# Optimization experiments

Hardware: AMD Instinct MI355X
Metric: run time of the kernel (lower is better)

## Reference

```python
import jax, jax.numpy as jnp
import numpy as np

WS = 8
NH = 16
EPS = 1e-5

# relative position index (static, same as the torch buffer)
def _rel_index(ws):
    coords = np.stack(np.meshgrid(np.arange(ws), np.arange(ws), indexing='ij'))  # 2,ws,ws
    flat = coords.reshape(2, -1)
    rel = flat[:, :, None] - flat[:, None, :]
    rel = rel.transpose(1, 2, 0).copy()
    rel[..., 0] += ws - 1
    rel[..., 1] += ws - 1
    rel[..., 0] *= 2 * ws - 1
    return rel.sum(-1)  # (ws*ws, ws*ws)

REL_IDX = jnp.asarray(_rel_index(WS))

def conv2d(x, w, dilation=1, pad=None, groups=1):
    k = w.shape[-1]
    if pad is None:
        pad = (dilation * (k - 1)) // 2
    return jax.lax.conv_general_dilated(
        x, w, (1, 1), ((pad, pad), (pad, pad)), rhs_dilation=(dilation, dilation),
        dimension_numbers=('NCHW', 'OIHW', 'NCHW'), feature_group_count=groups)

def bn(x, p):
    g, b, m, v = p[0], p[1], p[2], p[3]
    inv = g / jnp.sqrt(v + EPS)
    return x * inv[:, None, None] + (b - m * inv)[:, None, None]

def avgpool(x, kh, kw, ph, pw):
    # torch AvgPool2d with count_include_pad=True: zero-pad then divide by kernel size
    s = jax.lax.reduce_window(x, 0.0, jax.lax.add, (1, 1, kh, kw), (1, 1, 1, 1),
                              ((0, 0), (0, 0), (ph, ph), (pw, pw)))
    return s / (kh * kw)

def _fwd(x, w_pre, bn_pre, w_l1, bn_l1, w_l2, bn_l2, w_l3, bn_l3, w_qkv, rpb, w_dw, w_pw, bn_proj):
    B, C, H, W = x.shape
    # local conv branch (chunk 256 -> 86,86,84 with dilations 1,2,3)
    local = bn(conv2d(x, w_pre), bn_pre)
    l1 = bn(conv2d(local[:, :86], w_l1, dilation=1), bn_l1)
    l2 = bn(conv2d(local[:, 86:172], w_l2, dilation=2), bn_l2)
    l3 = bn(conv2d(local[:, 172:], w_l3, dilation=3), bn_l3)
    local = jnp.concatenate([l1, l2, l3], axis=1)
    # pad to window multiple (reflect); static shapes so Python branch is fine
    ph, pw = (-H) % WS, (-W) % WS
    if ph or pw:
        x = jnp.pad(x, ((0, 0), (0, 0), (0, ph), (0, pw)), mode='reflect')
    Hp, Wp = H + ph, W + pw
    hh, ww = Hp // WS, Wp // WS
    d = C // NH
    qkv = conv2d(x, w_qkv)  # (B, 3C, Hp, Wp)
    qkv = qkv.reshape(B, 3, NH, d, hh, WS, ww, WS)
    qkv = qkv.transpose(1, 0, 4, 6, 2, 5, 7, 3).reshape(3, B * hh * ww, NH, WS * WS, d)
    q, k, v = qkv[0], qkv[1], qkv[2]
    dots = jnp.einsum('whid,whjd->whij', q, k) * (d ** -0.5)
    bias = rpb[REL_IDX.reshape(-1)].reshape(WS * WS, WS * WS, NH).transpose(2, 0, 1)
    attn = jax.nn.softmax(dots + bias[None], axis=-1)
    out = jnp.einsum('whij,whjd->whid', attn, v)
    out = out.reshape(B, hh, ww, NH, WS, WS, d).transpose(0, 3, 6, 1, 4, 2, 5).reshape(B, C, Hp, Wp)
    out = out[:, :, :H, :W]
    ax = avgpool(jnp.pad(out, ((0, 0), (0, 0), (0, 1), (0, 0)), mode='reflect'), WS, 1, WS // 2 - 1, 0)
    ay = avgpool(jnp.pad(out, ((0, 0), (0, 0), (0, 0), (0, 1)), mode='reflect'), 1, WS, 0, WS // 2 - 1)
    out = ax + ay + local
    out = jnp.pad(out, ((0, 0), (0, 0), (0, 1), (0, 1)), mode='reflect')
    out = conv2d(out, w_dw, pad=3, groups=C)       # depthwise 8x8
    out = bn(conv2d(out, w_pw), bn_proj)           # pointwise + BN
    return out[:, :, :H, :W]

def setup_inputs() -> dict:
    key = jax.random.key(0)
    ks = jax.random.split(key, 16)
    def w(k, shape, s=0.05):
        return jax.random.normal(k, shape, dtype=jnp.float32) * s
    def bnp(k, c):
        p = jax.random.uniform(k, (4, c), dtype=jnp.float32)
        return p.at[3].add(0.5)  # keep var positive and away from 0
    return {
        'x': jax.random.normal(ks[0], (8, 256, 128, 128), dtype=jnp.float32),
        'w_pre': w(ks[1], (256, 256, 1, 1)), 'bn_pre': bnp(ks[2], 256),
        'w_l1': w(ks[3], (86, 86, 3, 3)), 'bn_l1': bnp(ks[4], 86),
        'w_l2': w(ks[5], (86, 86, 3, 3)), 'bn_l2': bnp(ks[6], 86),
        'w_l3': w(ks[7], (84, 84, 3, 3)), 'bn_l3': bnp(ks[8], 84),
        'w_qkv': w(ks[9], (768, 256, 1, 1)),
        'rpb': w(ks[10], (225, 16), 0.02),
        'w_dw': w(ks[11], (256, 1, 8, 8)),
        'w_pw': w(ks[12], (256, 256, 1, 1)),
        'bn_proj': bnp(ks[13], 256),
    }

def reference(x, w_pre, bn_pre, w_l1, bn_l1, w_l2, bn_l2, w_l3, bn_l3, w_qkv, rpb, w_dw, w_pw, bn_proj):
    return _fwd(x, w_pre, bn_pre, w_l1, bn_l1, w_l2, bn_l2, w_l3, bn_l3, w_qkv, rpb, w_dw, w_pw, bn_proj)
```

## Files before the change

### kernel.cpp

```cpp
#include <hip/hip_runtime.h>
#include <hip/hip_bf16.h>
#include <cstdint>
#include <cstddef>

namespace {

constexpr int HW = 16384;

typedef short vec8s __attribute__((ext_vector_type(8)));
typedef float f32x4 __attribute__((ext_vector_type(4)));

__device__ __forceinline__ float u2f(uint32_t u){ union { uint32_t u; float f; } v; v.u = u; return v.f; }
__device__ __forceinline__ uint32_t f2u(float f){ union { float f; uint32_t u; } v; v.f = f; return v.u; }
__device__ __forceinline__ uint16_t f2bf(float f){
  uint32_t u = f2u(f);
  u += 0x7fffu + ((u >> 16) & 1u);
  return (uint16_t)(u >> 16);
}
__device__ __forceinline__ void unpack2(uint32_t w, float& lo, float& hi){
  lo = u2f(w << 16);
  hi = u2f(w & 0xffff0000u);
}

__global__ __launch_bounds__(256) void k_cast(
    const float* __restrict__ x, uint16_t* __restrict__ xT)
{
  __shared__ float sF[64][129];
  const int t = threadIdx.x;
  const int b = blockIdx.x >> 7;
  const int y = blockIdx.x & 127;
  const size_t rowoff = (size_t)y * 128;
  for (int cc = 0; cc < 4; ++cc) {
    const int cic0 = cc * 64;
    #pragma unroll
    for (int k = 0; k < 8; ++k) {
      int e = t + k * 256;
      int ci = e >> 5;
      int pxq = (e & 31) * 4;
      float4 v = *(const float4*)(x + (size_t)(b * 256 + cic0 + ci) * HW + rowoff + pxq);
      sF[ci][pxq] = v.x; sF[ci][pxq+1] = v.y; sF[ci][pxq+2] = v.z; sF[ci][pxq+3] = v.w;
    }
    __syncthreads();
    {
      int px = t >> 1, h = t & 1;
      __align__(16) uint16_t tmp[32];
      #pragma unroll
      for (int j = 0; j < 32; ++j) tmp[j] = f2bf(sF[h * 32 + j][px]);
      uint16_t* dst = xT + ((size_t)b * HW + rowoff + px) * 256 + cic0 + h * 32;
      *(uint4*)(dst)      = *(uint4*)&tmp[0];
      *(uint4*)(dst + 8)  = *(uint4*)&tmp[8];
      *(uint4*)(dst + 16) = *(uint4*)&tmp[16];
      *(uint4*)(dst + 24) = *(uint4*)&tmp[24];
    }
    __syncthreads();
  }
}

template<int OUT_MODE, int NCO>
__global__ __launch_bounds__(256) void k_gemm_v2(
    const uint16_t* __restrict__ xT, const float* __restrict__ wmat,
    const float* __restrict__ bnp, int M,
    uint16_t* __restrict__ outb, float* __restrict__ outf)
{
  __shared__ __align__(16) uint16_t sX[128][260];
  __shared__ __align__(16) uint16_t sW[128][36];
  const int t = threadIdx.x;
  const int b    = blockIdx.x >> 7;
  const int tile = blockIdx.x & 127;
  const int l = t & 63, w = t >> 6;
  const int l15 = l & 15, koct = l >> 4;
  const int wc = w >> 1, wp = w & 1;

  {
    const int spx = t >> 1, sh = t & 1;
    int gpx;
    if constexpr (OUT_MODE == 3) {
      int win = tile * 2 + (spx >> 6);
      int p = spx & 63;
      gpx = ((win >> 4) * 8 + (p >> 3)) * 128 + (win & 15) * 8 + (p & 7);
    } else {
      gpx = tile * 128 + spx;
    }
    const uint16_t* src = xT + ((size_t)b * HW + gpx) * 256 + sh * 128;
    uint16_t* dst = &sX[spx][sh * 128];
    #pragma unroll
    for (int i = 0; i < 16; ++i)
      *(uint4*)(dst + i * 8) = *(const uint4*)(src + i * 8);
  }

  const int swc = t >> 1, swh = t & 1;
  float4 wr0, wr1, wr2, wr3;
  {
    const float* p = wmat + (size_t)swc * 256 + swh * 16;
    wr0 = *(const float4*)(p);     wr1 = *(const float4*)(p + 4);
    wr2 = *(const float4*)(p + 8); wr3 = *(const float4*)(p + 12);
  }
  __syncthreads();

  for (int cc = 0; cc < NCO; ++cc) {
    f32x4 acc[4][4];
    #pragma unroll
    for (int cf = 0; cf < 4; ++cf)
      #pragma unroll
      for (int pf = 0; pf < 4; ++pf) acc[cf][pf] = (f32x4){0.f,0.f,0.f,0.f};

    for (int kc = 0; kc < 8; ++kc) {
      if (cc | kc) __syncthreads();
      {
        __align__(16) uint16_t tmp[16];
        tmp[0]=f2bf(wr0.x); tmp[1]=f2bf(wr0.y); tmp[2]=f2bf(wr0.z); tmp[3]=f2bf(wr0.w);
        tmp[4]=f2bf(wr1.x); tmp[5]=f2bf(wr1.y); tmp[6]=f2bf(wr1.z); tmp[7]=f2bf(wr1.w);
        tmp[8]=f2bf(wr2.x); tmp[9]=f2bf(wr2.y); tmp[10]=f2bf(wr2.z); tmp[11]=f2bf(wr2.w);
        tmp[12]=f2bf(wr3.x); tmp[13]=f2bf(wr3.y); tmp[14]=f2bf(wr3.z); tmp[15]=f2bf(wr3.w);
        uint16_t* dst = &sW[swc][swh * 16];
        *(uint4*)(dst)     = *(uint4*)&tmp[0];
        *(uint4*)(dst + 8) = *(uint4*)&tmp[8];
      }
      {
        int nkc = kc + 1, ncc = cc;
        if (nkc == 8) { nkc = 0; ncc = cc + 1; }
        if (ncc < NCO) {
          const float* p = wmat + (size_t)(ncc * 128 + swc) * 256 + nkc * 32 + swh * 16;
          wr0 = *(const float4*)(p);     wr1 = *(const float4*)(p + 4);
          wr2 = *(const float4*)(p + 8); wr3 = *(const float4*)(p + 12);
        }
      }
      __syncthreads();
      vec8s bf[4];
      #pragma unroll
      for (int pf = 0; pf < 4; ++pf)
        bf[pf] = *(const vec8s*)&sX[wp * 64 + pf * 16 + l15][kc * 32 + koct * 8];
      #pragma unroll
      for (int cf = 0; cf < 4; ++cf) {
        vec8s af = *(const vec8s*)&sW[wc * 64 + cf * 16 + l15][koct * 8];
        #pragma unroll
        for (int pf = 0; pf < 4; ++pf)
          acc[cf][pf] = __builtin_amdgcn_mfma_f32_16x16x32_bf16(af, bf[pf], acc[cf][pf], 0, 0, 0);
      }
    }

    #pragma unroll
    for (int cf = 0; cf < 4; ++cf) {
      const int cbase = cc * 128 + wc * 64 + cf * 16 + koct * 4;
      float scv[4], shv[4];
      #pragma unroll
      for (int r = 0; r < 4; ++r) {
        scv[r] = 1.f; shv[r] = 0.f;
        if constexpr (OUT_MODE == 0 || OUT_MODE == 2) {
          int c = cbase + r;
          float g = bnp[c], be = bnp[M + c], mu = bnp[2 * M + c], va = bnp[3 * M + c];
          scv[r] = g * rsqrtf(va + 1e-5f);
          shv[r] = be - mu * scv[r];
        }
      }
      #pragma unroll
      for (int pf = 0; pf < 4; ++pf) {
        if constexpr (OUT_MODE == 0) {
          int px = tile * 128 + wp * 64 + pf * 16 + l15;
          __align__(8) uint16_t pk[4];
          #pragma unroll
          for (int r = 0; r < 4; ++r)
            pk[r] = f2bf(fmaf(acc[cf][pf][r], scv[r], shv[r]));
          *(uint2*)(outb + ((size_t)b * HW + px) * 256 + cbase) = *(uint2*)pk;
        } else if constexpr (OUT_MODE == 2) {
          int px = tile * 128 + wp * 64 + pf * 16 + l15;
          #pragma unroll
          for (int r = 0; r < 4; ++r)
            outf[(size_t)(b * M + cbase + r) * HW + px] =
                fmaf(acc[cf][pf][r], scv[r], shv[r]);
        } else {
          int win = tile * 2 + wp;
          int p = pf * 16 + l15;
          uint16_t* dstp = outb + ((size_t)(b * 256 + win) * 768 + cbase) * 64 + p;
          #pragma unroll
          for (int r = 0; r < 4; ++r)
            dstp[(size_t)r * 64] = f2bf(acc[cf][pf][r]);
        }
      }
    }
  }
}

template<int DIL, int CG>
__global__ __launch_bounds__(256) void k_dilconv_mfma(
    const uint16_t* __restrict__ preT, const float* __restrict__ wt,
    const float* __restrict__ bnp, float* __restrict__ out,
    int cb, int cb_al)
{
  constexpr int R = 8 + 2 * DIL;
  constexpr int C = 64 + 2 * DIL;
  constexpr int NPOS = R * C;
  constexpr int NIT = (NPOS + 255) / 256;
  __shared__ __align__(16) uint16_t sX[NPOS * 16];
  __shared__ __align__(16) uint16_t sW[10 * 50 * 16];

  const int t = threadIdx.x;
  const int rt    = blockIdx.x >> 1;
  const int ctile = blockIdx.x & 1;
  const int ct2   = blockIdx.y;
  const int b     = blockIdx.z;
  const int y0 = rt * 8, x0 = ctile * 64;
  const int l = t & 63, w = t >> 6;
  const int l15 = l & 15, oct = (l >> 4) & 1, half = l >> 5;
  const int rbase = w * 2;

  f32x4 acc[3][8];
  #pragma unroll
  for (int cf = 0; cf < 3; ++cf)
    #pragma unroll
    for (int q = 0; q < 8; ++q) acc[cf][q] = (f32x4){0.f,0.f,0.f,0.f};

  for (int kc = 0; kc < 6; ++kc) {
    #pragma unroll
    for (int i = 0; i < 3; ++i) {
      int pair = t + i * 256;
      int co = pair >> 4, ci = pair & 15;
      int cog = ct2 * 48 + co;
      int c = cb_al + kc * 16 + ci;
      bool ok = (cog < CG) && (c >= cb) && (c < cb + CG);
      size_t widx = ok ? ((size_t)cog * (size_t)CG + (size_t)(c - cb)) * 9u
                       : (size_t)0;
      const float* wp = wt + widx;
      uint16_t* dst = &sW[co * 16 + ci];
      #pragma unroll
      for (int tap = 0; tap < 9; ++tap)
        dst[tap * 800] = ok ? f2bf(wp[tap]) : (uint16_t)0;
      dst[9 * 800] = 0;
    }
    #pragma unroll
    for (int i = 0; i < NIT; ++i) {
      int p = t + i * 256;
      if (p < NPOS) {
        int row = p / C, col = p % C;
        int gy = y0 + row - DIL, gx = x0 + col - DIL;
        uint4 va = {0,0,0,0}, vb = {0,0,0,0};
        if ((unsigned)gy < 128u && (unsigned)gx < 128u) {
          const uint4* src = (const uint4*)(preT +
              (((size_t)b * HW + gy * 128 + gx) * 256 + cb_al + kc * 16));
          va = src[0]; vb = src[1];
        }
        uint4* dst = (uint4*)&sX[p * 16];
        dst[0] = va; dst[1] = vb;
      }
    }
    __syncthreads();

    #pragma unroll
    for (int s = 0; s < 5; ++s) {
      const int tap0 = 2 * s, tap1 = 2 * s + 1;
      const int dy0 = tap0 / 3, dx0 = tap0 % 3;
      const int dy1 = (tap1 <= 8) ? tap1 / 3 : 2;
      const int dx1 = (tap1 <= 8) ? tap1 % 3 : 2;
      const int dy = half ? dy1 : dy0;
      const int dx = half ? dx1 : dx0;
      const int atap = tap0 + half;
      vec8s a0 = *(const vec8s*)&sW[(atap * 50 + 0  + l15) * 16 + oct * 8];
      vec8s a1 = *(const vec8s*)&sW[(atap * 50 + 16 + l15) * 16 + oct * 8];
      vec8s a2 = *(const vec8s*)&sW[(atap * 50 + 32 + l15) * 16 + oct * 8];
      #pragma unroll
      for (int rs = 0; rs < 2; ++rs) {
        const int rowin = rbase + rs + dy * DIL;
        #pragma unroll
        for (int c4 = 0; c4 < 4; ++c4) {
          const int colin = c4 * 16 + l15 + dx * DIL;
          vec8s bf = *(const vec8s*)&sX[(rowin * C + colin) * 16 + oct * 8];
          acc[0][rs*4+c4] = __builtin_amdgcn_mfma_f32_16x16x32_bf16(a0, bf, acc[0][rs*4+c4], 0, 0, 0);
          acc[1][rs*4+c4] = __builtin_amdgcn_mfma_f32_16x16x32_bf16(a1, bf, acc[1][rs*4+c4], 0, 0, 0);
          acc[2][rs*4+c4] = __builtin_amdgcn_mfma_f32_16x16x32_bf16(a2, bf, acc[2][rs*4+c4], 0, 0, 0);
        }
      }
    }
    __syncthreads();
  }

  const int row4 = (l >> 4);
  #pragma unroll
  for (int cf = 0; cf < 3; ++cf) {
    #pragma unroll
    for (int r = 0; r < 4; ++r) {
      int c_loc = ct2 * 48 + cf * 16 + row4 * 4 + r;
      if (c_loc < CG) {
        int cg = cb + c_loc;
        float g = bnp[c_loc], be = bnp[CG + c_loc];
        float mu = bnp[2 * CG + c_loc], va = bnp[3 * CG + c_loc];
        float scv = g * rsqrtf(va + 1e-5f);
        float shv = be - mu * scv;
        #pragma unroll
        for (int rs = 0; rs < 2; ++rs) {
          int y = y0 + rbase + rs;
          #pragma unroll
          for (int c4 = 0; c4 < 4; ++c4) {
            int x = x0 + c4 * 16 + l15;
            out[(size_t)(b * 256 + cg) * HW + y * 128 + x] =
                fmaf(acc[cf][rs*4+c4][r], scv, shv);
          }
        }
      }
    }
  }
}

__global__ __launch_bounds__(256) void k_attn(
    const uint16_t* __restrict__ qkvW, const float* __restrict__ rpb,
    uint16_t* __restrict__ outp)
{
  __shared__ __align__(16) uint16_t sAll[4][9928];
  const int t = threadIdx.x;
  const int l = t & 63, w = t >> 6;
  const int l15 = l & 15, koct = l >> 4;
  const int b = blockIdx.y;
  const int win = blockIdx.x;
  const int wy = win >> 4, wx = win & 15;
  const int wbase = (wy * 8) * 128 + wx * 8;
  const uint16_t* base = qkvW + (size_t)(b * 256 + win) * 49152;
  uint16_t* swKT = &sAll[w][0];
  uint16_t* swQT = &sAll[w][2560];
  uint16_t* swPT = &sAll[w][5120];
  float*    swB  = (float*)&sAll[w][9472];
  float*    swO  = (float*)swPT;

  {
    uint4 z = {0,0,0,0};
    *(uint4*)(swKT + l * 40 + 16) = z;
    *(uint4*)(swKT + l * 40 + 24) = z;
    *(uint4*)(swQT + l * 40 + 16) = z;
    *(uint4*)(swQT + l * 40 + 24) = z;
  }

  for (int it = 0; it < 4; ++it) {
    const int n = w + it * 4;
    #pragma unroll
    for (int m = 0; m < 4; ++m) {
      int e = l + m * 64;
      if (e < 225) swB[e] = rpb[e * 16 + n];
    }
    const uint16_t* qg = base + (size_t)(n * 16) * 64;
    const uint16_t* kg = base + (size_t)(256 + n * 16) * 64;
    const uint16_t* vg = base + (size_t)(512 + n * 16) * 64;
    {
      uint32_t kp[8], qp[8];
      #pragma unroll
      for (int m = 0; m < 8; ++m) {
        uint32_t k0 = kg[(2 * m) * 64 + l], k1 = kg[(2 * m + 1) * 64 + l];
        uint32_t q0 = qg[(2 * m) * 64 + l], q1 = qg[(2 * m + 1) * 64 + l];
        kp[m] = k0 | (k1 << 16);
        qp[m] = q0 | (q1 << 16);
      }
      *(uint4*)(swKT + l * 40)     = *(uint4*)&kp[0];
      *(uint4*)(swKT + l * 40 + 8) = *(uint4*)&kp[4];
      *(uint4*)(swQT + l * 40)     = *(uint4*)&qp[0];
      *(uint4*)(swQT + l * 40 + 8) = *(uint4*)&qp[4];
    }
    asm volatile("s_waitcnt lgkmcnt(0)" ::: "memory");
    __builtin_amdgcn_sched_barrier(0);

    vec8s aK[4], bQ[4];
    #pragma unroll
    for (int tt = 0; tt < 4; ++tt) {
      aK[tt] = *(const vec8s*)(swKT + (tt * 16 + l15) * 40 + koct * 8);
      bQ[tt] = *(const vec8s*)(swQT + (tt * 16 + l15) * 40 + koct * 8);
    }
    f32x4 accS[4][4];
    #pragma unroll
    for (int ti = 0; ti < 4; ++ti)
      #pragma unroll
      for (int tj = 0; tj < 4; ++tj)
        accS[ti][tj] = __builtin_amdgcn_mfma_f32_16x16x32_bf16(
            aK[tj], bQ[ti], (f32x4){0.f, 0.f, 0.f, 0.f}, 0, 0, 0);

    float p[4][16], sinv[4];
    #pragma unroll
    for (int ti = 0; ti < 4; ++ti) {
      const int i = ti * 16 + l15;
      const int irow = i >> 3, icol = i & 7;
      #pragma unroll
      for (int tj = 0; tj < 4; ++tj) {
        #pragma unroll
        for (int r = 0; r < 4; ++r) {
          int j = tj * 16 + koct * 4 + r;
          int rel = (irow - (j >> 3) + 7) * 15 + (icol - (j & 7) + 7);
          p[ti][tj * 4 + r] = fmaf(accS[ti][tj][r], 0.25f, swB[rel]);
        }
      }
      float mx = p[ti][0];
      #pragma unroll
      for (int u = 1; u < 16; ++u) mx = fmaxf(mx, p[ti][u]);
      mx = fmaxf(mx, __shfl_xor(mx, 16));
      mx = fmaxf(mx, __shfl_xor(mx, 32));
      float s = 0.f;
      #pragma unroll
      for (int u = 0; u < 16; ++u) { p[ti][u] = __expf(p[ti][u] - mx); s += p[ti][u]; }
      s += __shfl_xor(s, 16);
      s += __shfl_xor(s, 32);
      sinv[ti] = 1.f / s;
    }

    #pragma unroll
    for (int ti = 0; ti < 4; ++ti) {
      uint16_t* rowp = swPT + (ti * 16 + l15) * 68 + koct * 4;
      #pragma unroll
      for (int tj = 0; tj < 4; ++tj) {
        uint32_t u0 = (uint32_t)f2bf(p[ti][tj * 4 + 0]) | ((uint32_t)f2bf(p[ti][tj * 4 + 1]) << 16);
        uint32_t u1 = (uint32_t)f2bf(p[ti][tj * 4 + 2]) | ((uint32_t)f2bf(p[ti][tj * 4 + 3]) << 16);
        *(uint32_t*)(rowp + tj * 16)     = u0;
        *(uint32_t*)(rowp + tj * 16 + 2) = u1;
      }
    }
    asm volatile("s_waitcnt lgkmcnt(0)" ::: "memory");
    __builtin_amdgcn_sched_barrier(0);

    f32x4 accO[4];
    #pragma unroll
    for (int ii = 0; ii < 4; ++ii) accO[ii] = (f32x4){0.f, 0.f, 0.f, 0.f};
    #pragma unroll
    for (int ks = 0; ks < 2; ++ks) {
      vec8s aV = *(const vec8s*)(vg + l15 * 64 + ks * 32 + koct * 8);
      #pragma unroll
      for (int ii = 0; ii < 4; ++ii) {
        vec8s bP;
        const uint16_t* src = swPT + (ii * 16 + l15) * 68 + ks * 32 + koct * 8;
        *(uint2*)&bP         = *(const uint2*)(src);
        *((uint2*)&bP + 1)   = *(const uint2*)(src + 4);
        accO[ii] = __builtin_amdgcn_mfma_f32_16x16x32_bf16(aV, bP, accO[ii], 0, 0, 0);
      }
    }
    asm volatile("s_waitcnt lgkmcnt(0)" ::: "memory");
    __builtin_amdgcn_sched_barrier(0);

    #pragma unroll
    for (int ii = 0; ii < 4; ++ii) {
      #pragma unroll
      for (int r = 0; r < 4; ++r) {
        int dd = koct * 4 + r;
        swO[dd * 76 + ii * 16 + l15] = accO[ii][r] * sinv[ii];
      }
    }
    asm volatile("s_waitcnt lgkmcnt(0)" ::: "memory");
    __builtin_amdgcn_sched_barrier(0);
    #pragma unroll
    for (int e2 = 0; e2 < 2; ++e2) {
      int e = l + e2 * 64;
      int dd = e >> 3, row = e & 7;
      const float* orow = swO + dd * 76 + row * 8;
      float4 a = *(const float4*)(orow);
      float4 c = *(const float4*)(orow + 4);
      uint4 pk;
      pk.x = (uint32_t)f2bf(a.x) | ((uint32_t)f2bf(a.y) << 16);
      pk.y = (uint32_t)f2bf(a.z) | ((uint32_t)f2bf(a.w) << 16);
      pk.z = (uint32_t)f2bf(c.x) | ((uint32_t)f2bf(c.y) << 16);
      pk.w = (uint32_t)f2bf(c.z) | ((uint32_t)f2bf(c.w) << 16);
      *(uint4*)(outp + (size_t)(b * 256 + n * 16 + dd) * HW + wbase + row * 128) = pk;
    }
    asm volatile("s_waitcnt lgkmcnt(0)" ::: "memory");
    __builtin_amdgcn_sched_barrier(0);
  }
}

__global__ __launch_bounds__(256) void k_pool(
    const uint16_t* __restrict__ attnb, float* __restrict__ loc)
{
  __shared__ __align__(16) float sP[71][136];
  const int t = threadIdx.x;
  const int plane = blockIdx.x >> 1;
  const int h0 = (blockIdx.x & 1) * 64;
  const size_t pbase = (size_t)plane * HW;
  #pragma unroll
  for (int k = 0; k < 5; ++k) {
    int idx = t + k * 256;
    if (idx < 71 * 16) {
      int lr = idx >> 4, m = idx & 15;
      int g = h0 - 3 + lr;
      float f[8] = {0.f,0.f,0.f,0.f,0.f,0.f,0.f,0.f};
      if (g >= 0 && g <= 127) {
        uint4 v4 = *(const uint4*)(attnb + pbase + (size_t)g * 128 + m * 8);
        unpack2(v4.x, f[0], f[1]); unpack2(v4.y, f[2], f[3]);
        unpack2(v4.z, f[4], f[5]); unpack2(v4.w, f[6], f[7]);
      }
      float* dst = &sP[lr][4 + m * 8];
      *(float4*)dst       = (float4){f[0], f[1], f[2], f[3]};
      *(float4*)(dst + 4) = (float4){f[4], f[5], f[6], f[7]};
    }
  }
  #pragma unroll
  for (int k = 0; k < 3; ++k) {
    int idx = t + k * 256;
    if (idx < 71 * 8) {
      int lr = idx >> 3, e = idx & 7;
      int c = (e < 4) ? e : (128 + e);
      sP[lr][c] = 0.f;
    }
  }
  __syncthreads();

  const int q  = t & 31;
  const int r0 = (t >> 5) * 8;
  const int w0 = q * 4;
  float4 av = {0.f, 0.f, 0.f, 0.f};
  #pragma unroll
  for (int o = 0; o < 8; ++o) {
    float4 v = *(const float4*)&sP[r0 + o][4 + w0];
    av.x += v.x; av.y += v.y; av.z += v.z; av.w += v.w;
  }
  #pragma unroll
  for (int rr = 0; rr < 8; ++rr) {
    const int lh = r0 + rr;
    const int h = h0 + lh;
    float4 a = av;
    if (h >= 124) {
      float4 cfix = *(const float4*)&sP[126 - 64 + 3][4 + w0];
      a.x += cfix.x; a.y += cfix.y; a.z += cfix.z; a.w += cfix.w;
    }
    float4 hv0 = *(const float4*)&sP[lh + 3][w0];
    float4 hv1 = *(const float4*)&sP[lh + 3][w0 + 4];
    float4 hv2 = *(const float4*)&sP[lh + 3][w0 + 8];
    float s0 = hv0.y + hv0.z + hv0.w + hv1.x + hv1.y + hv1.z + hv1.w + hv2.x;
    float s1 = s0 - hv0.y + hv2.y;
    float s2 = s1 - hv0.z + hv2.z;
    float s3 = s2 - hv0.w + hv2.w;
    if (q == 31) {
      float cfix = sP[lh + 3][130];
      s0 += cfix; s1 += cfix; s2 += cfix; s3 += cfix;
    }
    const size_t gi = pbase + (size_t)h * 128 + w0;
    float4 lv = *(const float4*)(loc + gi);
    float4 o4;
    o4.x = fmaf(a.x + s0, 0.125f, lv.x);
    o4.y = fmaf(a.y + s1, 0.125f, lv.y);
    o4.z = fmaf(a.z + s2, 0.125f, lv.z);
    o4.w = fmaf(a.w + s3, 0.125f, lv.w);
    *(float4*)(loc + gi) = o4;
    if (rr < 7) {
      float4 vm = *(const float4*)&sP[lh][4 + w0];
      float4 vp = *(const float4*)&sP[lh + 8][4 + w0];
      av.x += vp.x - vm.x; av.y += vp.y - vm.y;
      av.z += vp.z - vm.z; av.w += vp.w - vm.w;
    }
  }
}

__global__ __launch_bounds__(256) void k_dw(
    const float* __restrict__ comb, const float* __restrict__ wdw,
    float* __restrict__ out)
{
  __shared__ __align__(16) float sZ[71][136];
  __shared__ float sWd[64];
  const int t = threadIdx.x;
  const int plane = blockIdx.x >> 1;
  const int cch = plane & 255;
  const int h0 = (blockIdx.x & 1) * 64;
  const size_t pbase = (size_t)plane * HW;
  if (t < 64) sWd[t] = wdw[cch * 64 + t];
  #pragma unroll
  for (int k = 0; k < 5; ++k) {
    int idx = t + k * 256;
    if (idx < 71 * 16) {
      int lr = idx >> 4, m = idx & 15;
      int g = h0 - 3 + lr;
      float4 a = {0.f,0.f,0.f,0.f}, c = {0.f,0.f,0.f,0.f};
      if (g >= 0 && g <= 128) {
        int gr = (g == 128) ? 126 : g;
        const float* src = comb + pbase + (size_t)gr * 128 + m * 8;
        a = *(const float4*)(src);
        c = *(const float4*)(src + 4);
      }
      float* dst = &sZ[lr][4 + m * 8];
      *(float4*)dst       = a;
      *(float4*)(dst + 4) = c;
    }
  }
  if (t < 71) {
    int lr = t;
    int g = h0 - 3 + lr;
    float rv = 0.f;
    if (g >= 0 && g <= 128) {
      int gr = (g == 128) ? 126 : g;
      rv = comb[pbase + (size_t)gr * 128 + 126];
    }
    *(float4*)&sZ[lr][0] = (float4){0.f, 0.f, 0.f, 0.f};
    sZ[lr][132] = rv;
    sZ[lr][133] = 0.f; sZ[lr][134] = 0.f; sZ[lr][135] = 0.f;
  }
  __syncthreads();

  float wt[8][8];
  #pragma unroll
  for (int i = 0; i < 8; ++i) {
    *(float4*)&wt[i][0] = *(const float4*)&sWd[i * 8];
    *(float4*)&wt[i][4] = *(const float4*)&sWd[i * 8 + 4];
  }

  const int q  = t & 31;
  const int rg = t >> 5;
  const int w0 = q * 4;
  f32x4 acc[8];
  #pragma unroll
  for (int rr = 0; rr < 8; ++rr) acc[rr] = (f32x4){0.f,0.f,0.f,0.f};

  #pragma unroll
  for (int v = 0; v < 15; ++v) {
    const int lr = rg * 8 + v;
    float win[12];
    *(float4*)&win[0] = *(const float4*)&sZ[lr][w0];
    *(float4*)&win[4] = *(const float4*)&sZ[lr][w0 + 4];
    *(float4*)&win[8] = *(const float4*)&sZ[lr][w0 + 8];
    #pragma unroll
    for (int rr = 0; rr < 8; ++rr) {
      const int i = v - rr;
      if (i >= 0 && i < 8) {
        #pragma unroll
        for (int c = 0; c < 4; ++c) {
          float s = acc[rr][c];
          #pragma unroll
          for (int j = 0; j < 8; ++j)
            s = fmaf(wt[i][j], win[c + j + 1], s);
          acc[rr][c] = s;
        }
      }
    }
  }
  #pragma unroll
  for (int rr = 0; rr < 8; ++rr) {
    int h = h0 + rg * 8 + rr;
    float* dst = out + pbase + (size_t)h * 128 + w0;
    *(float4*)dst = (float4){acc[rr][0], acc[rr][1], acc[rr][2], acc[rr][3]};
  }
}

}

extern "C" void kernel_launch(void* const* d_in, const int* in_sizes, int n_in,
                              void* d_out, int out_size, void* d_ws, size_t ws_size,
                              hipStream_t stream)
{
  const float* x      = (const float*)d_in[0];
  const float* w_pre  = (const float*)d_in[1];
  const float* bn_pre = (const float*)d_in[2];
  const float* w_l1   = (const float*)d_in[3];
  const float* bn_l1  = (const float*)d_in[4];
  const float* w_l2   = (const float*)d_in[5];
  const float* bn_l2  = (const float*)d_in[6];
  const float* w_l3   = (const float*)d_in[7];
  const float* bn_l3  = (const float*)d_in[8];
  const float* w_qkv  = (const float*)d_in[9];
  const float* rpb    = (const float*)d_in[10];
  const float* w_dw   = (const float*)d_in[11];
  const float* w_pw   = (const float*)d_in[12];
  const float* bn_pj  = (const float*)d_in[13];
  float* out = (float*)d_out;

  char* base = (char*)d_ws;
  uint16_t* xT    = (uint16_t*)base;
  uint16_t* preT  = (uint16_t*)(base + (size_t)67108864);
  float*    bufB  = (float*)(base + (size_t)134217728);
  uint16_t* bufQ  = (uint16_t*)(base + (size_t)268435456);
  uint16_t* attnO = preT;
  float*    bufDw = (float*)bufQ;
  uint16_t* dwT   = xT;

  dim3 blk(256);
  k_cast<<<dim3(1024), blk, 0, stream>>>(x, xT);
  k_gemm_v2<0, 2><<<dim3(1024), blk, 0, stream>>>(xT, w_pre, bn_pre, 256, preT, nullptr);
  k_dilconv_mfma<1, 86><<<dim3(32, 2, 8), blk, 0, stream>>>(preT, w_l1, bn_l1, bufB, 0, 0);
  k_dilconv_mfma<2, 86><<<dim3(32, 2, 8), blk, 0, stream>>>(preT, w_l2, bn_l2, bufB, 86, 80);
  k_dilconv_mfma<3, 84><<<dim3(32, 2, 8), blk, 0, stream>>>(preT, w_l3, bn_l3, bufB, 172, 160);
  k_gemm_v2<3, 6><<<dim3(1024), blk, 0, stream>>>(xT, w_qkv, nullptr, 768, bufQ, nullptr);
  k_attn<<<dim3(256, 8), blk, 0, stream>>>(bufQ, rpb, attnO);
  k_pool<<<dim3(4096), blk, 0, stream>>>(attnO, bufB);
  k_dw<<<dim3(4096), blk, 0, stream>>>(bufB, w_dw, bufDw);
  k_cast<<<dim3(1024), blk, 0, stream>>>(bufDw, dwT);
  k_gemm_v2<2, 2><<<dim3(1024), blk, 0, stream>>>(dwT, w_pw, bn_pj, 256, nullptr, out);

  (void)in_sizes; (void)n_in; (void)out_size; (void)ws_size;
}
```

Measured before the change: 761.2 us.

## Pre-convert 1x1 conv weights to bf16 and read MFMA operands from global

Adds a small kernel that casts the pre, qkv and projection 1x1 weights to bf16 once per call, storing them in scratch space (the output buffer and a freed workspace region). The GEMM kernel then loads its A fragments straight from global/L2 instead of staging converted weights through shared memory. This removes the per-k-step conversion, the shared-memory writes and two barriers per k-chunk, so the inner loop runs without synchronisation. In exchange, every wave issues its own redundant global loads of weights, relying on cache hits, and there are extra small launches.

```diff
diff --git a/kernel.cpp b/kernel.cpp
--- a/kernel.cpp
+++ b/kernel.cpp
@@ -20,6 +20,22 @@
 __device__ __forceinline__ void unpack2(uint32_t w, float& lo, float& hi){
   lo = u2f(w << 16);
   hi = u2f(w & 0xffff0000u);
+}
+
+__global__ __launch_bounds__(256) void k_w2bf(
+    const float* __restrict__ src, uint16_t* __restrict__ dst, int n)
+{
+  int i = (blockIdx.x * 256 + threadIdx.x) * 8;
+  if (i + 8 <= n) {
+    float4 a = *(const float4*)(src + i);
+    float4 b = *(const float4*)(src + i + 4);
+    uint4 pk;
+    pk.x = (uint32_t)f2bf(a.x) | ((uint32_t)f2bf(a.y) << 16);
+    pk.y = (uint32_t)f2bf(a.z) | ((uint32_t)f2bf(a.w) << 16);
+    pk.z = (uint32_t)f2bf(b.x) | ((uint32_t)f2bf(b.y) << 16);
+    pk.w = (uint32_t)f2bf(b.z) | ((uint32_t)f2bf(b.w) << 16);
+    *(uint4*)(dst + i) = pk;
+  }
 }
 
 __global__ __launch_bounds__(256) void k_cast(
@@ -57,13 +73,12 @@
 }
 
 template<int OUT_MODE, int NCO>
-__global__ __launch_bounds__(256) void k_gemm_v2(
-    const uint16_t* __restrict__ xT, const float* __restrict__ wmat,
+__global__ __launch_bounds__(256) void k_gemm_v3(
+    const uint16_t* __restrict__ xT, const uint16_t* __restrict__ wbf,
     const float* __restrict__ bnp, int M,
     uint16_t* __restrict__ outb, float* __restrict__ outf)
 {
   __shared__ __align__(16) uint16_t sX[128][260];
-  __shared__ __align__(16) uint16_t sW[128][36];
   const int t = threadIdx.x;
   const int b    = blockIdx.x >> 7;
   const int tile = blockIdx.x & 127;
@@ -87,14 +102,6 @@
     for (int i = 0; i < 16; ++i)
       *(uint4*)(dst + i * 8) = *(const uint4*)(src + i * 8);
   }
-
-  const int swc = t >> 1, swh = t & 1;
-  float4 wr0, wr1, wr2, wr3;
-  {
-    const float* p = wmat + (size_t)swc * 256 + swh * 16;
-    wr0 = *(const float4*)(p);     wr1 = *(const float4*)(p + 4);
-    wr2 = *(const float4*)(p + 8); wr3 = *(const float4*)(p + 12);
-  }
   __syncthreads();
 
   for (int cc = 0; cc < NCO; ++cc) {
@@ -104,35 +111,16 @@
       #pragma unroll
       for (int pf = 0; pf < 4; ++pf) acc[cf][pf] = (f32x4){0.f,0.f,0.f,0.f};
 
+    const uint16_t* wbase = wbf + (size_t)(cc * 128 + wc * 64 + l15) * 256 + koct * 8;
+    #pragma unroll
     for (int kc = 0; kc < 8; ++kc) {
-      if (cc | kc) __syncthreads();
-      {
-        __align__(16) uint16_t tmp[16];
-        tmp[0]=f2bf(wr0.x); tmp[1]=f2bf(wr0.y); tmp[2]=f2bf(wr0.z); tmp[3]=f2bf(wr0.w);
-        tmp[4]=f2bf(wr1.x); tmp[5]=f2bf(wr1.y); tmp[6]=f2bf(wr1.z); tmp[7]=f2bf(wr1.w);
-        tmp[8]=f2bf(wr2.x); tmp[9]=f2bf(wr2.y); tmp[10]=f2bf(wr2.z); tmp[11]=f2bf(wr2.w);
-        tmp[12]=f2bf(wr3.x); tmp[13]=f2bf(wr3.y); tmp[14]=f2bf(wr3.z); tmp[15]=f2bf(wr3.w);
-        uint16_t* dst = &sW[swc][swh * 16];
-        *(uint4*)(dst)     = *(uint4*)&tmp[0];
-        *(uint4*)(dst + 8) = *(uint4*)&tmp[8];
-      }
-      {
-        int nkc = kc + 1, ncc = cc;
-        if (nkc == 8) { nkc = 0; ncc = cc + 1; }
-        if (ncc < NCO) {
-          const float* p = wmat + (size_t)(ncc * 128 + swc) * 256 + nkc * 32 + swh * 16;
-          wr0 = *(const float4*)(p);     wr1 = *(const float4*)(p + 4);
-          wr2 = *(const float4*)(p + 8); wr3 = *(const float4*)(p + 12);
-        }
-      }
-      __syncthreads();
       vec8s bf[4];
       #pragma unroll
       for (int pf = 0; pf < 4; ++pf)
         bf[pf] = *(const vec8s*)&sX[wp * 64 + pf * 16 + l15][kc * 32 + koct * 8];
       #pragma unroll
       for (int cf = 0; cf < 4; ++cf) {
-        vec8s af = *(const vec8s*)&sW[wc * 64 + cf * 16 + l15][koct * 8];
+        vec8s af = *(const vec8s*)(wbase + (size_t)(cf * 16) * 256 + kc * 32);
         #pragma unroll
         for (int pf = 0; pf < 4; ++pf)
           acc[cf][pf] = __builtin_amdgcn_mfma_f32_16x16x32_bf16(af, bf[pf], acc[cf][pf], 0, 0, 0);
@@ -656,19 +644,25 @@
   uint16_t* attnO = preT;
   float*    bufDw = (float*)bufQ;
   uint16_t* dwT   = xT;
+  uint16_t* wpre_bf = (uint16_t*)out;
+  uint16_t* wqkv_bf = wpre_bf + 65536;
+  uint16_t* wpw_bf  = preT;
 
   dim3 blk(256);
+  k_w2bf<<<dim3(32),  blk, 0, stream>>>(w_pre, wpre_bf, 65536);
+  k_w2bf<<<dim3(96),  blk, 0, stream>>>(w_qkv, wqkv_bf, 196608);
   k_cast<<<dim3(1024), blk, 0, stream>>>(x, xT);
-  k_gemm_v2<0, 2><<<dim3(1024), blk, 0, stream>>>(xT, w_pre, bn_pre, 256, preT, nullptr);
+  k_gemm_v3<0, 2><<<dim3(1024), blk, 0, stream>>>(xT, wpre_bf, bn_pre, 256, preT, nullptr);
   k_dilconv_mfma<1, 86><<<dim3(32, 2, 8), blk, 0, stream>>>(preT, w_l1, bn_l1, bufB, 0, 0);
   k_dilconv_mfma<2, 86><<<dim3(32, 2, 8), blk, 0, stream>>>(preT, w_l2, bn_l2, bufB, 86, 80);
   k_dilconv_mfma<3, 84><<<dim3(32, 2, 8), blk, 0, stream>>>(preT, w_l3, bn_l3, bufB, 172, 160);
-  k_gemm_v2<3, 6><<<dim3(1024), blk, 0, stream>>>(xT, w_qkv, nullptr, 768, bufQ, nullptr);
+  k_gemm_v3<3, 6><<<dim3(1024), blk, 0, stream>>>(xT, wqkv_bf, nullptr, 768, bufQ, nullptr);
   k_attn<<<dim3(256, 8), blk, 0, stream>>>(bufQ, rpb, attnO);
   k_pool<<<dim3(4096), blk, 0, stream>>>(attnO, bufB);
+  k_w2bf<<<dim3(32), blk, 0, stream>>>(w_pw, wpw_bf, 65536);
   k_dw<<<dim3(4096), blk, 0, stream>>>(bufB, w_dw, bufDw);
   k_cast<<<dim3(1024), blk, 0, stream>>>(bufDw, dwT);
-  k_gemm_v2<2, 2><<<dim3(1024), blk, 0, stream>>>(dwT, w_pw, bn_pj, 256, nullptr, out);
+  k_gemm_v3<2, 2><<<dim3(1024), blk, 0, stream>>>(dwT, wpw_bf, bn_pj, 256, nullptr, out);
 
   (void)in_sizes; (void)n_in; (void)out_size; (void)ws_size;
 }
```

New measurement: 839.3 us. +10.3%, slower.
